# Kernel tuning notes

Measured on AMD Instinct MI355X. Metric: run time of the kernel, lower is better.

Reference implementation:

```python
import jax, jax.numpy as jnp
import numpy as np

B, L, D_NODE, D_EDGE, H = 4, 256, 256, 128, 8
DK = D_NODE // H        # 32, per-head node dim
DE = D_EDGE // H        # 16, per-head edge dim
NEG_SLOPE = 0.2

# Static index maps replicating the torch loop indexing (including its j-1 off-by-one / wraparound bug)
_GIDX = np.arange(L - 1)[None, :] + (np.arange(L - 1)[None, :] >= np.arange(L)[:, None])  # [L, L-1]: j-values visited for row i (j != i, in order)
_PIDX = (np.arange(L) - 1) % (L - 1)   # [L]: torch uses attention_probs[:, j-1] for every j != i
_II = np.arange(L)[:, None]            # [L, 1]


def lrelu(x):
    return jnp.where(x >= 0, x, NEG_SLOPE * x)


def setup_inputs() -> dict:
    key = jax.random.key(0)
    ks = jax.random.split(key, 19)
    w = lambda k, s, sc=0.05: jax.random.normal(k, s, jnp.float32) * sc
    return dict(
        node=w(ks[0], (B, L, D_NODE), 1.0),
        edge=w(ks[1], (B, L, L, D_EDGE), 1.0),
        Wn_w=w(ks[2], (D_NODE, D_NODE)), Wn_b=w(ks[3], (D_NODE,)),
        Wh_w=w(ks[4], (DK, DK)), Wh_b=w(ks[5], (DK,)),
        We_w=w(ks[6], (D_EDGE, D_EDGE)), We_b=w(ks[7], (D_EDGE,)),
        Wn2_w=w(ks[8], (D_NODE, D_NODE)), Wn2_b=w(ks[9], (D_NODE,)),
        We2_w=w(ks[10], (D_EDGE, D_EDGE)), We2_b=w(ks[11], (D_EDGE,)),
        attn_w=w(ks[12], (2 * DK + DE,)),                  # attn_linear (no bias), input order [hi, hj, eij]
        edge_w=w(ks[13], (DE + 2 * DK, DE)), edge_b=w(ks[14], (DE,)),  # edge_linear, input order [eij, hi, hj]
        out_n_w=w(ks[15], (D_NODE, D_NODE)), out_n_b=w(ks[16], (D_NODE,)),
        out_e_w=w(ks[17], (D_EDGE, D_EDGE)), out_e_b=w(ks[18], (D_EDGE,)),
    )


def reference(node, edge, Wn_w, Wn_b, Wh_w, Wh_b, We_w, We_b, Wn2_w, Wn2_b,
              We2_w, We2_b, attn_w, edge_w, edge_b, out_n_w, out_n_b, out_e_w, out_e_b):
    node_p = (node @ Wn_w + Wn_b).reshape(B, L, H, DK)
    edge_p = (edge @ We_w + We_b).reshape(B, L, L, H, DE)

    # ---- node update (all heads at once) ----
    wq, wk, we = attn_w[:DK], attn_w[DK:2 * DK], attn_w[2 * DK:]
    si = jnp.einsum('bihd,d->bih', node_p, wq)
    sj = jnp.einsum('bjhd,d->bjh', node_p, wk)
    se = jnp.einsum('bijhd,d->bijh', edge_p, we)
    scores = si[:, :, None, :] + sj[:, None, :, :] + se          # [B,L,L,H], score(i,j)
    sc = scores[:, _II, _GIDX, :]                                 # [B,L,L-1,H]: j != i, loop order
    probs = jax.nn.softmax(lrelu(sc), axis=2)                     # softmax over the L-1 neighbors
    probs_pair = probs[:, :, _PIDX, :]                            # [B,L,L,H]: replicate probs[:, j-1]
    mask = (1.0 - jnp.eye(L, dtype=node.dtype))[None, :, :, None]
    Whh = jnp.einsum('bjhd,de->bjhe', node_p, Wh_w) + Wh_b        # Wh(hj), bias inside the sum
    agg = jnp.einsum('bijh,bjhe->bihe', probs_pair * mask, Whh)
    node_h = (node_p + lrelu(agg)).reshape(B, L, D_NODE)          # concat heads == reshape
    new_node = node_h @ out_n_w + out_n_b

    # ---- edge update ----
    node_p2 = (new_node @ Wn2_w + Wn2_b).reshape(B, L, H, DK)
    edge_p2 = (edge @ We2_w + We2_b).reshape(B, L, L, H, DE)
    w_e, w_i, w_j = edge_w[:DE], edge_w[DE:DE + DK], edge_w[DE + DK:]
    e_new = (jnp.einsum('bijhd,de->bijhe', edge_p2, w_e)
             + jnp.einsum('bihd,de->bihe', node_p2, w_i)[:, :, None]
             + jnp.einsum('bjhd,de->bjhe', node_p2, w_j)[:, None]
             + edge_b)
    e_new = e_new * mask[..., None]                               # diagonal stays zero (zeros_like init)
    new_edge = e_new.reshape(B, L, L, D_EDGE) @ out_e_w + out_e_b
    return new_node, new_edge
```

## Files before the change

### kernel.cpp

```cpp
#include <hip/hip_runtime.h>

#define Bb 4
#define Ll 256
#define NEG 0.2f

typedef __attribute__((ext_vector_type(8))) short short8;
typedef __attribute__((ext_vector_type(4))) float f32x4;
typedef __attribute__((ext_vector_type(4))) unsigned uint4v;

__device__ __forceinline__ float lrelu(float x) { return x >= 0.f ? x : NEG * x; }

__device__ __forceinline__ short f2bf(float x) {
  unsigned u = __builtin_bit_cast(unsigned, x);
  unsigned r = (u + 0x7FFFu + ((u >> 16) & 1u)) >> 16;
  return (short)r;
}

__device__ __forceinline__ unsigned pack2bf(float e, float o) {
  unsigned ue = __builtin_bit_cast(unsigned, e);
  unsigned uo = __builtin_bit_cast(unsigned, o);
  return ((ue + 0x8000u) >> 16) | ((uo + 0x8000u) & 0xFFFF0000u);
}

__global__ void prep_kernel(const float* We_w, const float* We_b, const float* attn_w,
                            const float* We2_w, const float* We2_b, const float* edge_w,
                            const float* edge_b, const float* out_e_w, const float* out_e_b,
                            float* Vg, float* chg, float* c0g, short* Gsw) {
  int blk = blockIdx.x;
  int t = threadIdx.x;
  if (blk < 128) {
    __shared__ float m2[128];
    int c = blk;
    int h = t >> 4, e = t & 15;
    float s = 0.f;
    for (int d = 0; d < 16; ++d) s += We2_w[c * 128 + h * 16 + d] * edge_w[d * 16 + e];
    m2[t] = s;
    __syncthreads();
    float g = 0.f;
    for (int f = 0; f < 128; ++f) g += m2[f] * out_e_w[f * 128 + t];
    int off = t * 256 + ((2 * c) ^ ((t & 7) << 4));
    *(short*)((char*)Gsw + off) = f2bf(g);
  } else {
    __shared__ float b2e[128];
    const float* we = attn_w + 64;
    for (int idx = t; idx < 1024; idx += 128) {
      int c = idx >> 3, h = idx & 7;
      float s = 0.f;
      for (int d = 0; d < 16; ++d) s += We_w[c * 128 + h * 16 + d] * we[d];
      Vg[idx] = s;
    }
    if (t < 8) {
      float s = 0.f;
      for (int d = 0; d < 16; ++d) s += We_b[t * 16 + d] * we[d];
      chg[t] = s;
    }
    {
      int h = t >> 4, e = t & 15;
      float s = 0.f;
      for (int d = 0; d < 16; ++d) s += We2_b[h * 16 + d] * edge_w[d * 16 + e];
      b2e[t] = s + edge_b[e];
    }
    __syncthreads();
    float s = out_e_b[t];
    for (int f = 0; f < 128; ++f) s += b2e[f] * out_e_w[f * 128 + t];
    c0g[t] = s;
  }
}

__global__ __launch_bounds__(256) void se_kernel(const float* __restrict__ edge,
                                                 const float* __restrict__ Vg,
                                                 const float* __restrict__ chg,
                                                 float* __restrict__ se) {
  int t = threadIdx.x;
  int l16 = t & 15;
  long gid = ((long)blockIdx.x * 256 + t) >> 4;
  long ngroups = ((long)gridDim.x * 256) >> 4;
  float vreg[8][8];
#pragma unroll
  for (int ci = 0; ci < 8; ++ci) {
    int c = (ci < 4) ? (l16 * 4 + ci) : (64 + l16 * 4 + (ci - 4));
#pragma unroll
    for (int h = 0; h < 8; ++h) vreg[ci][h] = Vg[c * 8 + h];
  }
  float chv = chg[(l16 >> 1) & 7];
  const long NR = (long)Bb * Ll * Ll;
  for (long row = gid; row < NR; row += ngroups) {
    const float4* er = reinterpret_cast<const float4*>(edge + row * 128);
    float4 e0 = er[l16];
    float4 e1 = er[16 + l16];
    float p[8];
#pragma unroll
    for (int h = 0; h < 8; ++h)
      p[h] = e0.x * vreg[0][h] + e0.y * vreg[1][h] + e0.z * vreg[2][h] + e0.w * vreg[3][h] +
             e1.x * vreg[4][h] + e1.y * vreg[5][h] + e1.z * vreg[6][h] + e1.w * vreg[7][h];
    bool hi8 = (l16 & 8) != 0;
    float q[4];
#pragma unroll
    for (int h = 0; h < 4; ++h) {
      float keep = hi8 ? p[h + 4] : p[h];
      float send = hi8 ? p[h] : p[h + 4];
      q[h] = keep + __shfl_xor(send, 8);
    }
    bool hi4 = (l16 & 4) != 0;
    float r2[2];
#pragma unroll
    for (int h = 0; h < 2; ++h) {
      float keep = hi4 ? q[h + 2] : q[h];
      float send = hi4 ? q[h] : q[h + 2];
      r2[h] = keep + __shfl_xor(send, 4);
    }
    bool hi2 = (l16 & 2) != 0;
    float s = (hi2 ? r2[1] : r2[0]) + __shfl_xor(hi2 ? r2[0] : r2[1], 2);
    s += __shfl_xor(s, 1);
    s += chv;
    if ((l16 & 1) == 0) se[row * 8 + ((l16 >> 1) & 7)] = s;
  }
}

__global__ __launch_bounds__(256) void node_in_fused(
    const float* __restrict__ node, const float* __restrict__ Wn_w,
    const float* __restrict__ Wn_b, const float* __restrict__ Wh_w,
    const float* __restrict__ Wh_b, const float* __restrict__ attn_w,
    float* __restrict__ node_p, float* __restrict__ Whh, float* __restrict__ si,
    float* __restrict__ sj) {
  __shared__ float a[4][256];
  __shared__ float np[4][256];
  int t = threadIdx.x;
  int row0 = blockIdx.x * 4;
  for (int q = t; q < 1024; q += 256) a[q >> 8][q & 255] = node[(long)row0 * 256 + q];
  __syncthreads();
  float acc[4];
  float bvv = Wn_b[t];
#pragma unroll
  for (int r = 0; r < 4; ++r) acc[r] = bvv;
  for (int k = 0; k < 256; ++k) {
    float w = Wn_w[k * 256 + t];
#pragma unroll
    for (int r = 0; r < 4; ++r) acc[r] += a[r][k] * w;
  }
#pragma unroll
  for (int r = 0; r < 4; ++r) {
    node_p[(long)(row0 + r) * 256 + t] = acc[r];
    np[r][t] = acc[r];
  }
  __syncthreads();
  int h = t >> 5, e = t & 31;
  float wb2 = Wh_b[e];
#pragma unroll
  for (int r = 0; r < 4; ++r) {
    float s = wb2;
    for (int d = 0; d < 32; ++d) s += np[r][h * 32 + d] * Wh_w[d * 32 + e];
    Whh[(long)(row0 + r) * 256 + t] = s;
  }
  if (t < 64) {
    int r = t >> 4, idx = t & 15, hh = idx & 7;
    const float* w = attn_w + (idx < 8 ? 0 : 32);
    float s = 0.f;
    for (int d = 0; d < 32; ++d) s += np[r][hh * 32 + d] * w[d];
    ((idx < 8) ? si : sj)[(long)(row0 + r) * 8 + hh] = s;
  }
}

__global__ __launch_bounds__(256) void attn_fused(
    const float* __restrict__ node_p, const float* __restrict__ Whh,
    const float* __restrict__ si, const float* __restrict__ sj,
    const float* __restrict__ seg, float* __restrict__ node_h) {
  __shared__ float sjl[2048];
  __shared__ float sel[2048];
  __shared__ float pl[2048];
  __shared__ float sil[8];
  int t = threadIdx.x, bi = blockIdx.x;
  int b = bi >> 8, i = bi & 255;
  for (int q = t; q < 2048; q += 256) sjl[q] = sj[(long)b * 2048 + q];
  for (int q = t; q < 2048; q += 256) sel[q] = seg[(long)bi * 2048 + q];
  if (t < 8) sil[t] = si[(long)bi * 8 + t];
  __syncthreads();

  int g = t >> 5, l32 = t & 31;
  float sc[8];
  float mx = -1e30f;
#pragma unroll
  for (int m = 0; m < 8; ++m) {
    int k = l32 + 32 * m;
    float v = -1e30f;
    if (k < 255) {
      int jj = k + (k >= i ? 1 : 0);
      v = sil[g] + sjl[jj * 8 + g] + sel[jj * 8 + g];
      v = lrelu(v);
    }
    sc[m] = v;
    mx = fmaxf(mx, v);
  }
#pragma unroll
  for (int d = 16; d >= 1; d >>= 1) mx = fmaxf(mx, __shfl_xor(mx, d));
  float sum = 0.f;
#pragma unroll
  for (int m = 0; m < 8; ++m) {
    int k = l32 + 32 * m;
    float e = (k < 255) ? __expf(sc[m] - mx) : 0.f;
    sc[m] = e;
    sum += e;
  }
#pragma unroll
  for (int d = 16; d >= 1; d >>= 1) sum += __shfl_xor(sum, d);
  float inv = 1.f / sum;
#pragma unroll
  for (int m = 0; m < 8; ++m) {
    int k = l32 + 32 * m;
    if (k < 255) pl[k * 8 + g] = sc[m] * inv;
  }
  __syncthreads();

  int h = g;
  const float* wb = Whh + (long)b * 65536 + t;
  float acc0 = 0.f, acc1 = 0.f;
#pragma unroll 8
  for (int j = 0; j < 256; j += 2) {
    int k0 = (j == 0) ? 254 : (j - 1);
    int k1 = j;
    float w0 = (j == i) ? 0.f : pl[k0 * 8 + h];
    float w1 = (j + 1 == i) ? 0.f : pl[k1 * 8 + h];
    acc0 += w0 * wb[(long)j * 256];
    acc1 += w1 * wb[(long)(j + 1) * 256];
  }
  float acc = acc0 + acc1;
  float np = node_p[(long)bi * 256 + t];
  node_h[(long)bi * 256 + t] = np + lrelu(acc);
}

__global__ __launch_bounds__(256) void node_out_pq(
    const float* __restrict__ node_h, const float* __restrict__ out_n_w,
    const float* __restrict__ out_n_b, const float* __restrict__ Wn2_w,
    const float* __restrict__ Wn2_b, const float* __restrict__ edge_w,
    const float* __restrict__ out_e_w, float* __restrict__ out_node,
    float* __restrict__ Pg, float* __restrict__ Qg) {
  __shared__ float a[4][256];
  __shared__ float b2[4][256];
  __shared__ float ninj[4][256];
  int t = threadIdx.x;
  int row0 = blockIdx.x * 4;
  for (int q = t; q < 1024; q += 256) a[q >> 8][q & 255] = node_h[(long)row0 * 256 + q];
  __syncthreads();
  float acc[4];
  float bv1 = out_n_b[t];
#pragma unroll
  for (int r = 0; r < 4; ++r) acc[r] = bv1;
  for (int k = 0; k < 256; ++k) {
    float w = out_n_w[k * 256 + t];
#pragma unroll
    for (int r = 0; r < 4; ++r) acc[r] += a[r][k] * w;
  }
#pragma unroll
  for (int r = 0; r < 4; ++r) {
    out_node[(long)(row0 + r) * 256 + t] = acc[r];
    b2[r][t] = acc[r];
  }
  __syncthreads();
  float acc2[4];
  float bv2 = Wn2_b[t];
#pragma unroll
  for (int r = 0; r < 4; ++r) acc2[r] = bv2;
  for (int k = 0; k < 256; ++k) {
    float w = Wn2_w[k * 256 + t];
#pragma unroll
    for (int r = 0; r < 4; ++r) acc2[r] += b2[r][k] * w;
  }
#pragma unroll
  for (int r = 0; r < 4; ++r) a[r][t] = acc2[r];
  __syncthreads();
  {
    int f = t & 127, h = f >> 4, e = f & 15;
    const float* w = edge_w + 256 + (t >> 7) * 512;
#pragma unroll
    for (int r = 0; r < 4; ++r) {
      float s = 0.f;
      for (int d = 0; d < 32; ++d) s += a[r][h * 32 + d] * w[d * 16 + e];
      ninj[r][t] = s;
    }
  }
  __syncthreads();
  {
    int o = t & 127;
    int half = (t >> 7) * 128;
#pragma unroll
    for (int r = 0; r < 4; ++r) {
      float s = 0.f;
      const float* src = ninj[r] + half;
      for (int f = 0; f < 128; ++f) s += src[f] * out_e_w[f * 128 + o];
      ((t < 128) ? Pg : Qg)[(long)(row0 + r) * 128 + o] = s;
    }
  }
}

__global__ __launch_bounds__(256) void edge_out_kernel(
    const float* __restrict__ edge, const short* __restrict__ Gsw,
    const float* __restrict__ Pg, const float* __restrict__ Qg,
    const float* __restrict__ c0g, const float* __restrict__ oeb,
    float* __restrict__ out_edge) {
  __shared__ __align__(16) char Gl[32768];
  int t = threadIdx.x;
  int w = t >> 6, l = t & 63;
  int lc = l & 15, lq = l >> 4;
  int blk = blockIdx.x;
  int bi = blk >> 1;
  int jh = (blk & 1) * 128;
  int b = bi >> 8, i = bi & 255;

  {
    const uint4v* gsrc = (const uint4v*)Gsw;
    uint4v* gdst = (uint4v*)Gl;
#pragma unroll
    for (int q = 0; q < 8; ++q) gdst[q * 256 + t] = gsrc[q * 256 + t];
  }
  float pcv[8], oebv[8];
#pragma unroll
  for (int nf = 0; nf < 8; ++nf) {
    int col = nf * 16 + lc;
    pcv[nf] = Pg[(long)bi * 128 + col] + c0g[col];
    oebv[nf] = oeb[col];
  }
  __syncthreads();

  const float* eslab = edge + (long)bi * 32768;
#pragma unroll
  for (int s = 0; s < 2; ++s) {
    int rowb = jh + w * 32 + s * 16;
    f32x4 acc[8];
#pragma unroll
    for (int nf = 0; nf < 8; ++nf) acc[nf] = (f32x4){0.f, 0.f, 0.f, 0.f};
#pragma unroll
    for (int ks = 0; ks < 4; ++ks) {
      const float* ap = eslab + (long)(rowb + lc) * 128 + ks * 32 + lq * 8;
      float4 f0 = *(const float4*)ap;
      float4 f1 = *(const float4*)(ap + 4);
      uint4v u;
      u.x = pack2bf(f0.x, f0.y);
      u.y = pack2bf(f0.z, f0.w);
      u.z = pack2bf(f1.x, f1.y);
      u.w = pack2bf(f1.z, f1.w);
      short8 av = __builtin_bit_cast(short8, u);
#pragma unroll
      for (int nf = 0; nf < 8; ++nf) {
        int col = nf * 16 + lc;
        short8 bvv =
            *(const short8*)(Gl + col * 256 + ((ks * 64 + lq * 16) ^ ((col & 7) << 4)));
        acc[nf] = __builtin_amdgcn_mfma_f32_16x16x32_bf16(av, bvv, acc[nf], 0, 0, 0);
      }
    }
#pragma unroll
    for (int r = 0; r < 4; ++r) {
      int jloc = rowb + lq * 4 + r;
      float* orow = out_edge + ((long)bi * 256 + jloc) * 128;
      const float* Qrow = Qg + (long)(b * 256 + jloc) * 128;
      bool diag = (jloc == i);
#pragma unroll
      for (int nf = 0; nf < 8; ++nf) {
        int col = nf * 16 + lc;
        float v = diag ? oebv[nf] : (acc[nf][r] + pcv[nf] + Qrow[col]);
        orow[col] = v;
      }
    }
  }
}

extern "C" void kernel_launch(void* const* d_in, const int* in_sizes, int n_in,
                              void* d_out, int out_size, void* d_ws, size_t ws_size,
                              hipStream_t stream) {
  const float* node = (const float*)d_in[0];
  const float* edge = (const float*)d_in[1];
  const float* Wn_w = (const float*)d_in[2];
  const float* Wn_b = (const float*)d_in[3];
  const float* Wh_w = (const float*)d_in[4];
  const float* Wh_b = (const float*)d_in[5];
  const float* We_w = (const float*)d_in[6];
  const float* We_b = (const float*)d_in[7];
  const float* Wn2_w = (const float*)d_in[8];
  const float* Wn2_b = (const float*)d_in[9];
  const float* We2_w = (const float*)d_in[10];
  const float* We2_b = (const float*)d_in[11];
  const float* attn_w = (const float*)d_in[12];
  const float* edge_w = (const float*)d_in[13];
  const float* edge_b = (const float*)d_in[14];
  const float* out_n_w = (const float*)d_in[15];
  const float* out_n_b = (const float*)d_in[16];
  const float* out_e_w = (const float*)d_in[17];
  const float* out_e_b = (const float*)d_in[18];

  float* out_node = (float*)d_out;
  float* out_edge = ((float*)d_out) + 262144;

  float* ws = (float*)d_ws;
  float* node_p = ws;
  float* Whh    = ws + 262144;
  float* node_h = ws + 524288;
  float* si     = ws + 786432;
  float* sjv    = ws + 794624;
  float* Pg     = ws + 802816;
  float* Qg     = ws + 933888;
  float* chg    = ws + 1064960;
  float* c0g    = ws + 1065088;
  short* Gsw    = (short*)(ws + 1065216);
  float* Vg     = ws + 1073408;
  float* seg    = ws + 1074432;

  prep_kernel<<<129, 128, 0, stream>>>(We_w, We_b, attn_w, We2_w, We2_b, edge_w, edge_b,
                                       out_e_w, out_e_b, Vg, chg, c0g, Gsw);
  node_in_fused<<<256, 256, 0, stream>>>(node, Wn_w, Wn_b, Wh_w, Wh_b, attn_w, node_p, Whh,
                                         si, sjv);
  se_kernel<<<2048, 256, 0, stream>>>(edge, Vg, chg, seg);
  attn_fused<<<1024, 256, 0, stream>>>(node_p, Whh, si, sjv, seg, node_h);
  node_out_pq<<<256, 256, 0, stream>>>(node_h, out_n_w, out_n_b, Wn2_w, Wn2_b, edge_w,
                                       out_e_w, out_node, Pg, Qg);
  edge_out_kernel<<<2048, 256, 0, stream>>>(edge, Gsw, Pg, Qg, c0g, out_e_b, out_edge);
}
```

Measured before the change: 167.5 us.

## Pipeline edge tiles through LDS with async global_load_lds double buffering

Rewrites edge_out_kernel as a persistent loop over 8 tiles of 32 rows per block. It double-buffers edge rows into LDS with global_load_lds so the next tile's load overlaps the current MFMA and epilogue. The combined weight G is now stored unswizzled-transposed and held in registers, with the 4 waves split 2x2 over rows and columns instead of staging 32 KB of G in LDS per block. This aims to hide global memory latency on the large edge stream and cut per-block setup. In exchange it adds a manual vmcnt wait and barrier that must be exactly right, and halves the grid.

```diff
diff --git a/kernel.cpp b/kernel.cpp
--- a/kernel.cpp
+++ b/kernel.cpp
@@ -25,7 +25,7 @@
 __global__ void prep_kernel(const float* We_w, const float* We_b, const float* attn_w,
                             const float* We2_w, const float* We2_b, const float* edge_w,
                             const float* edge_b, const float* out_e_w, const float* out_e_b,
-                            float* Vg, float* chg, float* c0g, short* Gsw) {
+                            float* Vg, float* chg, float* c0g, short* Gt) {
   int blk = blockIdx.x;
   int t = threadIdx.x;
   if (blk < 128) {
@@ -38,8 +38,7 @@
     __syncthreads();
     float g = 0.f;
     for (int f = 0; f < 128; ++f) g += m2[f] * out_e_w[f * 128 + t];
-    int off = t * 256 + ((2 * c) ^ ((t & 7) << 4));
-    *(short*)((char*)Gsw + off) = f2bf(g);
+    Gt[t * 128 + c] = f2bf(g);
   } else {
     __shared__ float b2e[128];
     const float* we = attn_w + 64;
@@ -292,47 +291,75 @@
   }
 }
 
-__global__ __launch_bounds__(256) void edge_out_kernel(
-    const float* __restrict__ edge, const short* __restrict__ Gsw,
+#define TPB_E 8
+__global__ __launch_bounds__(256, 3) void edge_out_kernel(
+    const float* __restrict__ edge, const short* __restrict__ Gt,
     const float* __restrict__ Pg, const float* __restrict__ Qg,
     const float* __restrict__ c0g, const float* __restrict__ oeb,
     float* __restrict__ out_edge) {
-  __shared__ __align__(16) char Gl[32768];
+  __shared__ __align__(16) float abuf[2][32 * 128];
   int t = threadIdx.x;
-  int w = t >> 6, l = t & 63;
+  int l = t & 63, wid = t >> 6;
+  int wm = wid >> 1, wn = wid & 1;
   int lc = l & 15, lq = l >> 4;
-  int blk = blockIdx.x;
-  int bi = blk >> 1;
-  int jh = (blk & 1) * 128;
-  int b = bi >> 8, i = bi & 255;
-
-  {
-    const uint4v* gsrc = (const uint4v*)Gsw;
-    uint4v* gdst = (uint4v*)Gl;
-#pragma unroll
-    for (int q = 0; q < 8; ++q) gdst[q * 256 + t] = gsrc[q * 256 + t];
-  }
-  float pcv[8], oebv[8];
-#pragma unroll
-  for (int nf = 0; nf < 8; ++nf) {
-    int col = nf * 16 + lc;
-    pcv[nf] = Pg[(long)bi * 128 + col] + c0g[col];
-    oebv[nf] = oeb[col];
-  }
-  __syncthreads();
-
-  const float* eslab = edge + (long)bi * 32768;
-#pragma unroll
-  for (int s = 0; s < 2; ++s) {
-    int rowb = jh + w * 32 + s * 16;
-    f32x4 acc[8];
-#pragma unroll
-    for (int nf = 0; nf < 8; ++nf) acc[nf] = (f32x4){0.f, 0.f, 0.f, 0.f};
+
+  short8 bv[4][4];
+#pragma unroll
+  for (int ks = 0; ks < 4; ++ks)
+#pragma unroll
+    for (int nf = 0; nf < 4; ++nf)
+      bv[ks][nf] = *(const short8*)(Gt + (wn * 64 + nf * 16 + lc) * 128 + ks * 32 + lq * 8);
+
+  float oebv[4];
+#pragma unroll
+  for (int nf = 0; nf < 4; ++nf) oebv[nf] = oeb[wn * 64 + nf * 16 + lc];
+
+  long tile0 = (long)blockIdx.x * TPB_E;
+
+  auto stage = [&](int buf, long tile) {
+#pragma unroll
+    for (int q = 0; q < 4; ++q) {
+      int L = q * 256 + t;
+      int row = L >> 5, c4 = L & 31;
+      int scol = (c4 * 4) ^ ((row & 7) << 2);
+      const float* gp = edge + (tile * 32 + row) * 128 + scol;
+      char* lp = (char*)abuf[buf] + q * 4096 + wid * 1024;
+      __builtin_amdgcn_global_load_lds(
+          (const __attribute__((address_space(1))) unsigned*)gp,
+          (__attribute__((address_space(3))) unsigned*)lp, 16, 0, 0);
+    }
+  };
+
+  stage(0, tile0);
+  __syncthreads();
+
+  int cur = 0;
+  for (int tt = 0; tt < TPB_E; ++tt) {
+    long tile = tile0 + tt;
+    if (tt + 1 < TPB_E) stage(cur ^ 1, tile + 1);
+
+    int bi = (int)(tile >> 3);
+    int b = bi >> 8, i = bi & 255;
+    int row0loc = (int)(tile & 7) * 32;
+
+    float pcv[4];
+#pragma unroll
+    for (int nf = 0; nf < 4; ++nf) {
+      int col = wn * 64 + nf * 16 + lc;
+      pcv[nf] = Pg[(long)bi * 128 + col] + c0g[col];
+    }
+
+    const char* rbase = (const char*)abuf[cur] + (wm * 16 + lc) * 512;
+    int sw = ((wm * 16 + lc) & 7) << 4;
+
+    f32x4 acc[4];
+#pragma unroll
+    for (int nf = 0; nf < 4; ++nf) acc[nf] = (f32x4){0.f, 0.f, 0.f, 0.f};
 #pragma unroll
     for (int ks = 0; ks < 4; ++ks) {
-      const float* ap = eslab + (long)(rowb + lc) * 128 + ks * 32 + lq * 8;
-      float4 f0 = *(const float4*)ap;
-      float4 f1 = *(const float4*)(ap + 4);
+      int cb = ks * 128 + lq * 32;
+      float4 f0 = *(const float4*)(rbase + (cb ^ sw));
+      float4 f1 = *(const float4*)(rbase + ((cb + 16) ^ sw));
       uint4v u;
       u.x = pack2bf(f0.x, f0.y);
       u.y = pack2bf(f0.z, f0.w);
@@ -340,26 +367,28 @@
       u.w = pack2bf(f1.z, f1.w);
       short8 av = __builtin_bit_cast(short8, u);
 #pragma unroll
-      for (int nf = 0; nf < 8; ++nf) {
-        int col = nf * 16 + lc;
-        short8 bvv =
-            *(const short8*)(Gl + col * 256 + ((ks * 64 + lq * 16) ^ ((col & 7) << 4)));
-        acc[nf] = __builtin_amdgcn_mfma_f32_16x16x32_bf16(av, bvv, acc[nf], 0, 0, 0);
-      }
-    }
+      for (int nf = 0; nf < 4; ++nf)
+        acc[nf] = __builtin_amdgcn_mfma_f32_16x16x32_bf16(av, bv[ks][nf], acc[nf], 0, 0, 0);
+    }
+
 #pragma unroll
     for (int r = 0; r < 4; ++r) {
-      int jloc = rowb + lq * 4 + r;
+      int jloc = row0loc + wm * 16 + lq * 4 + r;
       float* orow = out_edge + ((long)bi * 256 + jloc) * 128;
       const float* Qrow = Qg + (long)(b * 256 + jloc) * 128;
       bool diag = (jloc == i);
 #pragma unroll
-      for (int nf = 0; nf < 8; ++nf) {
-        int col = nf * 16 + lc;
+      for (int nf = 0; nf < 4; ++nf) {
+        int col = wn * 64 + nf * 16 + lc;
         float v = diag ? oebv[nf] : (acc[nf][r] + pcv[nf] + Qrow[col]);
         orow[col] = v;
       }
     }
+
+    asm volatile("s_waitcnt vmcnt(16)" ::: "memory");
+    __builtin_amdgcn_s_barrier();
+    asm volatile("" ::: "memory");
+    cur ^= 1;
   }
 }
 
@@ -399,17 +428,17 @@
   float* Qg     = ws + 933888;
   float* chg    = ws + 1064960;
   float* c0g    = ws + 1065088;
-  short* Gsw    = (short*)(ws + 1065216);
+  short* Gt     = (short*)(ws + 1065216);
   float* Vg     = ws + 1073408;
   float* seg    = ws + 1074432;
 
   prep_kernel<<<129, 128, 0, stream>>>(We_w, We_b, attn_w, We2_w, We2_b, edge_w, edge_b,
-                                       out_e_w, out_e_b, Vg, chg, c0g, Gsw);
+                                       out_e_w, out_e_b, Vg, chg, c0g, Gt);
   node_in_fused<<<256, 256, 0, stream>>>(node, Wn_w, Wn_b, Wh_w, Wh_b, attn_w, node_p, Whh,
                                          si, sjv);
   se_kernel<<<2048, 256, 0, stream>>>(edge, Vg, chg, seg);
   attn_fused<<<1024, 256, 0, stream>>>(node_p, Whh, si, sjv, seg, node_h);
   node_out_pq<<<256, 256, 0, stream>>>(node_h, out_n_w, out_n_b, Wn2_w, Wn2_b, edge_w,
                                        out_e_w, out_node, Pg, Qg);
-  edge_out_kernel<<<2048, 256, 0, stream>>>(edge, Gsw, Pg, Qg, c0g, out_e_b, out_edge);
-}
+  edge_out_kernel<<<1024, 256, 0, stream>>>(edge, Gt, Pg, Qg, c0g, out_e_b, out_edge);
+}
```

Result: faster. 164.2 us (-2.0%).
